# Kernel tuning notes

Hardware: AMD Instinct MI355X
Metric: run time of the kernel (lower is better)

The kernel has to match this reference:

```python
import jax, jax.numpy as jnp
import numpy as np

B, C, H, W = 4, 256, 96, 96
FOUT = 32
HW = H * W
N = HW // 2  # inside/outside pixel counts (50/50 mask)


def setup_inputs() -> dict:
    key = jax.random.key(0)
    ks = jax.random.split(key, 6)
    f = jax.random.normal(ks[0], (B, C, H, W), dtype=jnp.float32)
    # deterministic alternating mask -> fixed N_in = N_out = HW/2 (jit-friendly)
    flat = (jnp.arange(HW) % 2).astype(jnp.float32)
    mask = jnp.broadcast_to(flat.reshape(1, 1, H, W), (B, 1, H, W))
    idx_in = jnp.nonzero(flat > 0.5, size=N)[0].astype(jnp.int32)   # mask == 1
    idx_out = jnp.nonzero(flat < 0.5, size=N)[0].astype(jnp.int32)  # mask == 0
    scale = 0.02
    Wq = jax.random.normal(ks[1], (FOUT, C), dtype=jnp.float32) * scale
    Wk = jax.random.normal(ks[2], (FOUT, C), dtype=jnp.float32) * scale
    Wv = jax.random.normal(ks[3], (C, C), dtype=jnp.float32) * scale
    bq = jnp.zeros((FOUT,), jnp.float32)
    bk = jnp.zeros((FOUT,), jnp.float32)
    bv = jnp.zeros((C,), jnp.float32)
    gamma = jax.random.uniform(ks[4], (1,), dtype=jnp.float32) + 0.25  # nonzero
    return {"f": f, "mask": mask, "idx_out": idx_out, "idx_in": idx_in,
            "Wq": Wq, "bq": bq, "Wk": Wk, "bk": bk, "Wv": Wv, "bv": bv,
            "gamma": gamma}


def reference(f, mask, idx_out, idx_in, Wq, bq, Wk, bk, Wv, bv, gamma):
    b, c, h, w = f.shape
    ff = f.reshape(b, c, h * w)              # (b, c, hw)
    f_out_pix = ff[:, :, idx_out]            # (b, c, Nout) gather outside pixels
    f_in_pix = ff[:, :, idx_in]              # (b, c, Nin)  gather inside pixels
    # 1x1 convs on gathered pixel sets == per-pixel linear projections
    q = jnp.einsum('oc,bcn->bon', Wq, f_out_pix) + bq[None, :, None]  # (b, fout, Nout)
    k = jnp.einsum('oc,bcn->bon', Wk, f_in_pix) + bk[None, :, None]   # (b, fout, Nin)
    v = jnp.einsum('dc,bcn->bdn', Wv, f_in_pix) + bv[None, :, None]   # (b, c, Nin)
    energy = jnp.einsum('boq,bok->bqk', q, k)       # (b, Nout, Nin)
    att = jax.nn.softmax(energy, axis=-1)
    r_v = jnp.einsum('bck,bqk->bcq', v, att)        # (b, c, Nout)
    ff2 = ff.at[:, :, idx_out].set(r_v)             # scatter write-back
    f_reshape = ff2.reshape(b, c, h, w)
    # NOTE: in torch, f_in aliases f's storage and is mutated by the scatter,
    # so f_in == f_reshape here. Reproduce that aliasing faithfully.
    f_out = f_reshape * (1.0 - mask) * gamma + f_reshape
    return (f_reshape, f_out)
```

## Files before the change

### kernel.cpp

```cpp
#include <hip/hip_runtime.h>
#include <math.h>

#define B_DIM    4
#define C_DIM    256
#define HW_DIM   9216
#define N_PIX    4608
#define FOUT_DIM 32
#define L2E      1.44269504f

typedef float  f32x4  __attribute__((ext_vector_type(4)));
typedef short  bf16x8 __attribute__((ext_vector_type(8)));

static __device__ __forceinline__ unsigned short f2bf(float x) {
    union { float f; unsigned int u; } v; v.f = x;
    unsigned int r = v.u + 0x7fffu + ((v.u >> 16) & 1u);
    return (unsigned short)(r >> 16);
}
static __device__ __forceinline__ float bf2f(unsigned short u) {
    union { unsigned int u; float f; } v; v.u = (unsigned int)u << 16; return v.f;
}

static __device__ __forceinline__ void gload_lds16(const unsigned short* g, unsigned short* l) {
    __builtin_amdgcn_global_load_lds(
        (const __attribute__((address_space(1))) void*)g,
        (__attribute__((address_space(3))) void*)l, 16, 0, 0);
}

__global__ void inv_init(int* __restrict__ inv) {
    int i = blockIdx.x * 256 + threadIdx.x;
    if (i < HW_DIM) inv[i] = -1;
}
__global__ void inv_scatter(const int* __restrict__ idx_out, int* __restrict__ inv) {
    int i = blockIdx.x * 256 + threadIdx.x;
    if (i < N_PIX) inv[idx_out[i]] = i;
}

__global__ __launch_bounds__(256) void gather_f(
    const float* __restrict__ f, const int* __restrict__ idx_out, const int* __restrict__ idx_in,
    unsigned short* __restrict__ Fo, unsigned short* __restrict__ Fi) {
    __shared__ float Fs[2][32][65];
    __shared__ int io[64], ii[64];
    const int t = threadIdx.x;
    const int n0 = blockIdx.x * 64, c0 = blockIdx.y * 32, b = blockIdx.z;
    if (t < 64) { io[t] = idx_out[n0 + t]; ii[t] = idx_in[n0 + t]; }
    __syncthreads();
    const float* fb = f + (size_t)b * C_DIM * HW_DIM;
    const int nn = t & 63, cg = t >> 6;
#pragma unroll
    for (int i = 0; i < 8; i++) {
        int c = cg * 8 + i;
        Fs[0][c][nn] = fb[(size_t)(c0 + c) * HW_DIM + io[nn]];
        Fs[1][c][nn] = fb[(size_t)(c0 + c) * HW_DIM + ii[nn]];
    }
    __syncthreads();
    for (int r = t; r < 2048; r += 256) {
        int n = r >> 5, c = r & 31;
        size_t o = ((size_t)(b * N_PIX + n0 + n)) * C_DIM + c0 + c;
        Fo[o] = f2bf(Fs[0][c][n]);
        Fi[o] = f2bf(Fs[1][c][n]);
    }
}

#define FSP 40
__global__ __launch_bounds__(256) void qk_proj_mfma(
    const unsigned short* __restrict__ Fo, const unsigned short* __restrict__ Fi,
    const float* __restrict__ Wq, const float* __restrict__ bq,
    const float* __restrict__ Wk, const float* __restrict__ bk,
    unsigned short* __restrict__ Q, unsigned short* __restrict__ K) {
    __shared__ unsigned short Ws[32 * 264];
    __shared__ unsigned short Fs[256 * FSP];
    const int t = threadIdx.x, n0 = blockIdx.x * 256, sel = blockIdx.y, b = blockIdx.z;
    const unsigned short* FX = sel ? Fi : Fo;
    const float* W    = sel ? Wk : Wq;
    const float* bias = sel ? bk : bq;
    unsigned short* O = sel ? K : Q;
#pragma unroll
    for (int j = 0; j < 8; j++) {
        int fid = j * 256 + t, row = fid >> 6, f4 = fid & 63;
        float4 wv = *(const float4*)(W + (size_t)row * C_DIM + f4 * 4);
        uint2 pk;
        pk.x = f2bf(wv.x) | ((unsigned)f2bf(wv.y) << 16);
        pk.y = f2bf(wv.z) | ((unsigned)f2bf(wv.w) << 16);
        *(uint2*)(Ws + row * 264 + f4 * 4) = pk;
    }
    const int w = t >> 6, l = t & 63, lq = l & 15, lg = l >> 4;
    f32x4 acc[8];
#pragma unroll
    for (int i = 0; i < 8; i++) acc[i] = (f32x4){0.f, 0.f, 0.f, 0.f};
    for (int cs = 0; cs < 8; cs++) {
        __syncthreads();
#pragma unroll
        for (int j = 0; j < 4; j++) {
            int cid = j * 256 + t, row = cid >> 2, ch = cid & 3;
            *(uint4*)(Fs + row * FSP + ch * 8) =
                *(const uint4*)(FX + ((size_t)(b * N_PIX + n0 + row)) * C_DIM + cs * 32 + ch * 8);
        }
        __syncthreads();
        bf16x8 bfr[2];
#pragma unroll
        for (int ob = 0; ob < 2; ob++)
            bfr[ob] = *(const bf16x8*)(Ws + (ob * 16 + lq) * 264 + cs * 32 + lg * 8);
#pragma unroll
        for (int ab = 0; ab < 4; ab++) {
            bf16x8 a = *(const bf16x8*)(Fs + (w * 64 + ab * 16 + lq) * FSP + lg * 8);
#pragma unroll
            for (int ob = 0; ob < 2; ob++)
                acc[ab * 2 + ob] = __builtin_amdgcn_mfma_f32_16x16x32_bf16(a, bfr[ob], acc[ab * 2 + ob], 0, 0, 0);
        }
    }
#pragma unroll
    for (int ab = 0; ab < 4; ab++)
#pragma unroll
        for (int ob = 0; ob < 2; ob++)
#pragma unroll
            for (int r = 0; r < 4; r++) {
                int n = n0 + w * 64 + ab * 16 + lg * 4 + r;
                int o = ob * 16 + lq;
                O[((size_t)(b * N_PIX + n)) * FOUT_DIM + o] = f2bf(acc[ab * 2 + ob][r] + bias[o]);
            }
}

__global__ __launch_bounds__(256) void v_proj_mfma(
    const unsigned short* __restrict__ Fi, const float* __restrict__ Wv,
    const float* __restrict__ bv, unsigned short* __restrict__ VT) {
    __shared__ unsigned short Ws[128 * FSP];
    __shared__ unsigned short Fs[128 * FSP];
    const int t = threadIdx.x, n0 = blockIdx.x * 128, d0 = blockIdx.y * 128, b = blockIdx.z;
    const int w = t >> 6, wd = w & 1, wn = w >> 1, l = t & 63, lq = l & 15, lg = l >> 4;
    f32x4 acc[16];
#pragma unroll
    for (int i = 0; i < 16; i++) acc[i] = (f32x4){0.f, 0.f, 0.f, 0.f};
    for (int cs = 0; cs < 8; cs++) {
        __syncthreads();
#pragma unroll
        for (int j = 0; j < 4; j++) {
            int row = j * 32 + (t >> 3), f4 = t & 7;
            float4 wv = *(const float4*)(Wv + (size_t)(d0 + row) * C_DIM + cs * 32 + f4 * 4);
            uint2 pk;
            pk.x = f2bf(wv.x) | ((unsigned)f2bf(wv.y) << 16);
            pk.y = f2bf(wv.z) | ((unsigned)f2bf(wv.w) << 16);
            *(uint2*)(Ws + row * FSP + f4 * 4) = pk;
        }
#pragma unroll
        for (int j = 0; j < 2; j++) {
            int cid = j * 256 + t, row = cid >> 2, ch = cid & 3;
            *(uint4*)(Fs + row * FSP + ch * 8) =
                *(const uint4*)(Fi + ((size_t)(b * N_PIX + n0 + row)) * C_DIM + cs * 32 + ch * 8);
        }
        __syncthreads();
        bf16x8 bfr[4];
#pragma unroll
        for (int nb = 0; nb < 4; nb++)
            bfr[nb] = *(const bf16x8*)(Fs + (wn * 64 + nb * 16 + lq) * FSP + lg * 8);
#pragma unroll
        for (int ab = 0; ab < 4; ab++) {
            bf16x8 a = *(const bf16x8*)(Ws + (wd * 64 + ab * 16 + lq) * FSP + lg * 8);
#pragma unroll
            for (int nb = 0; nb < 4; nb++)
                acc[ab * 4 + nb] = __builtin_amdgcn_mfma_f32_16x16x32_bf16(a, bfr[nb], acc[ab * 4 + nb], 0, 0, 0);
        }
    }
#pragma unroll
    for (int ab = 0; ab < 4; ab++)
#pragma unroll
        for (int r = 0; r < 4; r++) {
            int d = d0 + wd * 64 + ab * 16 + lg * 4 + r;
            float bvv = bv[d];
#pragma unroll
            for (int nb = 0; nb < 4; nb++) {
                int n = n0 + wn * 64 + nb * 16 + lq;
                VT[((size_t)(b * C_DIM + d)) * N_PIX + n] = f2bf(acc[ab * 4 + nb][r] + bvv);
            }
        }
}

__global__ __launch_bounds__(256, 2) void flash_attn(
    const unsigned short* __restrict__ Q, const unsigned short* __restrict__ K,
    const unsigned short* __restrict__ VT,
    unsigned short* __restrict__ Rpart, float* __restrict__ lpart) {
    __shared__ __align__(16) unsigned short VB[256 * 64];
    __shared__ __align__(16) unsigned short PB[2][32 * 72];
    __shared__ float lred[2][2][2][16];
    const int t = threadIdx.x, w = t >> 6, l = t & 63, lq = l & 15, lg = l >> 4;
    const int qg = w & 1, dh = w >> 1;
    const int bid = blockIdx.x;
    const int bz = bid & 7, b = bz & 3, ks = bz >> 2;
    const int q0 = (bid >> 3) * 64 + qg * 32;
    const int d0 = dh * 128;
    const unsigned short* Qb = Q + (size_t)b * N_PIX * FOUT_DIM;
    const unsigned short* Kb = K + (size_t)b * N_PIX * FOUT_DIM;
    const unsigned short* Vb = VT + (size_t)b * C_DIM * N_PIX;
    unsigned short* Rp = Rpart + (size_t)ks * 4718592;
    float* lp = lpart + ks * (B_DIM * N_PIX);

    bf16x8 qfr[2];
    qfr[0] = *(const bf16x8*)(Qb + (size_t)(q0 + lq) * 32 + lg * 8);
    qfr[1] = *(const bf16x8*)(Qb + (size_t)(q0 + 16 + lq) * 32 + lg * 8);

    f32x4 acc[2][8];
#pragma unroll
    for (int qb = 0; qb < 2; qb++)
#pragma unroll
        for (int db = 0; db < 8; db++) acc[qb][db] = (f32x4){0.f, 0.f, 0.f, 0.f};
    float lsum[2] = {0.f, 0.f};

    int voff[8];
#pragma unroll
    for (int j = 0; j < 8; j++) {
        int row = (w * 8 + j) * 8 + (l >> 3);
        int ch  = (l & 7) ^ (row & 7);
        voff[j] = row * N_PIX + ch * 8;
    }
    const int kt0 = ks * 36;
    bf16x8 kpf[2];
    {
        int kg = kt0 * 64;
#pragma unroll
        for (int j = 0; j < 8; j++)
            gload_lds16(Vb + voff[j] + kg, VB + (w * 8 + j) * 512);
#pragma unroll
        for (int kb = 0; kb < 2; kb++)
            kpf[kb] = *(const bf16x8*)(Kb + (size_t)(kg + dh * 32 + kb * 16 + lq) * 32 + lg * 8);
    }

    const int swz = lq & 7;
#pragma unroll 1
    for (int it = 0; it < 36; it++) {
        {
            const f32x4 z4 = {0.f, 0.f, 0.f, 0.f};
#pragma unroll
            for (int qb = 0; qb < 2; qb++) {
                f32x4 s[2];
#pragma unroll
                for (int kb = 0; kb < 2; kb++)
                    s[kb] = __builtin_amdgcn_mfma_f32_16x16x32_bf16(kpf[kb], qfr[qb], z4, 0, 0, 0);
                float ps = 0.f;
#pragma unroll
                for (int kb = 0; kb < 2; kb++) {
                    float p0 = exp2f(s[kb][0] * L2E);
                    float p1 = exp2f(s[kb][1] * L2E);
                    float p2 = exp2f(s[kb][2] * L2E);
                    float p3 = exp2f(s[kb][3] * L2E);
                    ps += (p0 + p1) + (p2 + p3);
                    unsigned int u0 = (__float_as_uint(p0) + 0x8000u) >> 16;
                    unsigned int u1 = (__float_as_uint(p1) + 0x8000u) & 0xffff0000u;
                    unsigned int u2 = (__float_as_uint(p2) + 0x8000u) >> 16;
                    unsigned int u3 = (__float_as_uint(p3) + 0x8000u) & 0xffff0000u;
                    uint2 pk; pk.x = u0 | u1; pk.y = u2 | u3;
                    *(uint2*)(PB[qg] + (qb * 16 + lq) * 72 + dh * 32 + kb * 16 + lg * 4) = pk;
                }
                lsum[qb] += ps;
            }
        }
        __syncthreads();
        if (it + 1 < 36) {
            int kn = (kt0 + it + 1) * 64;
#pragma unroll
            for (int kb = 0; kb < 2; kb++)
                kpf[kb] = *(const bf16x8*)(Kb + (size_t)(kn + dh * 32 + kb * 16 + lq) * 32 + lg * 8);
        }
        bf16x8 af[2][2];
#pragma unroll
        for (int qb = 0; qb < 2; qb++) {
            af[qb][0] = *(const bf16x8*)(PB[qg] + (qb * 16 + lq) * 72 + lg * 8);
            af[qb][1] = *(const bf16x8*)(PB[qg] + (qb * 16 + lq) * 72 + 32 + lg * 8);
        }
#pragma unroll
        for (int db = 0; db < 8; db++) {
            int row = d0 + db * 16 + lq;
            bf16x8 b0 = *(const bf16x8*)(VB + row * 64 + (lg ^ swz) * 8);
            bf16x8 b1 = *(const bf16x8*)(VB + row * 64 + ((lg + 4) ^ swz) * 8);
#pragma unroll
            for (int qb = 0; qb < 2; qb++) {
                acc[qb][db] = __builtin_amdgcn_mfma_f32_16x16x32_bf16(af[qb][0], b0, acc[qb][db], 0, 0, 0);
                acc[qb][db] = __builtin_amdgcn_mfma_f32_16x16x32_bf16(af[qb][1], b1, acc[qb][db], 0, 0, 0);
            }
        }
        __syncthreads();
        if (it + 1 < 36) {
            int kn = (kt0 + it + 1) * 64;
#pragma unroll
            for (int j = 0; j < 8; j++)
                gload_lds16(Vb + voff[j] + kn, VB + (w * 8 + j) * 512);
        }
    }
#pragma unroll
    for (int qb = 0; qb < 2; qb++)
#pragma unroll
        for (int r = 0; r < 4; r++) {
            int q = q0 + qb * 16 + lg * 4 + r;
            unsigned short* rp = Rp + ((size_t)(b * N_PIX + q)) * C_DIM + d0;
#pragma unroll
            for (int db = 0; db < 8; db++)
                rp[db * 16 + lq] = f2bf(acc[qb][db][r]);
        }
#pragma unroll
    for (int qb = 0; qb < 2; qb++) {
        float v = lsum[qb];
        v += __shfl_xor(v, 16);
        v += __shfl_xor(v, 32);
        if (l < 16) lred[dh][qg][qb][l] = v;
    }
    __syncthreads();
    if (dh == 0 && l < 16) {
#pragma unroll
        for (int qb = 0; qb < 2; qb++)
            lp[b * N_PIX + q0 + qb * 16 + l] = lred[0][qg][qb][l] + lred[1][qg][qb][l];
    }
}

__global__ __launch_bounds__(256) void epilogue(
    const float* __restrict__ f, const float* __restrict__ mask,
    const unsigned short* __restrict__ R0, const unsigned short* __restrict__ R1,
    const float* __restrict__ l0, const float* __restrict__ l1,
    const int* __restrict__ inv, const float* __restrict__ gamma,
    float* __restrict__ out0, float* __restrict__ out1) {
    const int gid = blockIdx.x * 256 + threadIdx.x;
    const size_t e = (size_t)gid * 4;
    const int p = (int)(e % HW_DIM);
    const int bc = (int)(e / HW_DIM);
    const int b = bc >> 8;
    const int c = bc & 255;
    const float g = gamma[0];
    float4 fv = *(const float4*)(f + e);
    const float* fvp = (const float*)&fv;
    float o0[4], o1[4];
#pragma unroll
    for (int u = 0; u < 4; u++) {
        int pp = p + u;
        int n = inv[pp];
        float val;
        if (n >= 0) {
            size_t ri = ((size_t)(b * N_PIX + n)) * C_DIM + c;
            float s = bf2f(R0[ri]) + bf2f(R1[ri]);
            val = s / (l0[b * N_PIX + n] + l1[b * N_PIX + n]);
        } else {
            val = fvp[u];
        }
        float mv = mask[b * HW_DIM + pp];
        o0[u] = val;
        o1[u] = val * (1.0f + g * (1.0f - mv));
    }
    *(float4*)(out0 + e) = make_float4(o0[0], o0[1], o0[2], o0[3]);
    *(float4*)(out1 + e) = make_float4(o1[0], o1[1], o1[2], o1[3]);
}

extern "C" void kernel_launch(void* const* d_in, const int* in_sizes, int n_in,
                              void* d_out, int out_size, void* d_ws, size_t ws_size,
                              hipStream_t stream) {
    const float* f       = (const float*)d_in[0];
    const float* mask    = (const float*)d_in[1];
    const int*   idx_out = (const int*)d_in[2];
    const int*   idx_in  = (const int*)d_in[3];
    const float* Wq      = (const float*)d_in[4];
    const float* bq      = (const float*)d_in[5];
    const float* Wk      = (const float*)d_in[6];
    const float* bk      = (const float*)d_in[7];
    const float* Wv      = (const float*)d_in[8];
    const float* bv      = (const float*)d_in[9];
    const float* gamma   = (const float*)d_in[10];

    unsigned short* ws   = (unsigned short*)d_ws;
    unsigned short* Fo   = ws;
    unsigned short* Fi   = ws + 4718592;
    unsigned short* VTw  = ws + 9437184;
    unsigned short* Qw   = ws + 14155776;
    unsigned short* Kw   = ws + 14745600;
    float*          lptr = (float*)(ws + 15335424);
    int*            inv  = (int*)(lptr + 2 * B_DIM * N_PIX);
    unsigned short* Rpart = Fo;

    float* out0 = (float*)d_out;
    float* out1 = out0 + (size_t)B_DIM * C_DIM * HW_DIM;

    inv_init<<<dim3(36), dim3(256), 0, stream>>>(inv);
    inv_scatter<<<dim3(18), dim3(256), 0, stream>>>(idx_out, inv);
    gather_f<<<dim3(72, 8, B_DIM), dim3(256), 0, stream>>>(f, idx_out, idx_in, Fo, Fi);
    qk_proj_mfma<<<dim3(18, 2, B_DIM), dim3(256), 0, stream>>>(Fo, Fi, Wq, bq, Wk, bk, Qw, Kw);
    v_proj_mfma<<<dim3(36, 2, B_DIM), dim3(256), 0, stream>>>(Fi, Wv, bv, VTw);
    flash_attn<<<dim3(576), dim3(256), 0, stream>>>(Qw, Kw, VTw, Rpart, lptr);
    epilogue<<<dim3(9216), dim3(256), 0, stream>>>(f, mask, Rpart, Rpart + 4718592,
                                                   lptr, lptr + B_DIM * N_PIX, inv, gamma, out0, out1);
}
```

Baseline: 285.5 us.

## Fuse Q/K/V projections and inverse-index build into one launch; vectorize gather stores

Merges the Q/K projection, V projection and inverse-index construction kernels into a single block-indexed 'prep' kernel, which cuts four launches down to one and lets the independent work run concurrently. The inverse-index init no longer fills the whole table with -1. It now writes -1 only at idx_in positions, which assumes idx_in and idx_out together cover every pixel. The gather kernel now writes 8 bf16 values per thread as one 16-byte store instead of scalar 2-byte stores. The trade-offs are a larger shared-memory footprint per block and branch divergence across block roles.

```diff
diff --git a/kernel.cpp b/kernel.cpp
--- a/kernel.cpp
+++ b/kernel.cpp
@@ -24,15 +24,6 @@
     __builtin_amdgcn_global_load_lds(
         (const __attribute__((address_space(1))) void*)g,
         (__attribute__((address_space(3))) void*)l, 16, 0, 0);
-}
-
-__global__ void inv_init(int* __restrict__ inv) {
-    int i = blockIdx.x * 256 + threadIdx.x;
-    if (i < HW_DIM) inv[i] = -1;
-}
-__global__ void inv_scatter(const int* __restrict__ idx_out, int* __restrict__ inv) {
-    int i = blockIdx.x * 256 + threadIdx.x;
-    if (i < N_PIX) inv[idx_out[i]] = i;
 }
 
 __global__ __launch_bounds__(256) void gather_f(
@@ -53,125 +44,142 @@
         Fs[1][c][nn] = fb[(size_t)(c0 + c) * HW_DIM + ii[nn]];
     }
     __syncthreads();
-    for (int r = t; r < 2048; r += 256) {
-        int n = r >> 5, c = r & 31;
-        size_t o = ((size_t)(b * N_PIX + n0 + n)) * C_DIM + c0 + c;
-        Fo[o] = f2bf(Fs[0][c][n]);
-        Fi[o] = f2bf(Fs[1][c][n]);
+    {
+        const int n = t >> 2, oc = (t & 3) * 8;
+        size_t o = ((size_t)(b * N_PIX + n0 + n)) * C_DIM + c0 + oc;
+        unsigned short tmp0[8], tmp1[8];
+#pragma unroll
+        for (int j = 0; j < 8; j++) {
+            tmp0[j] = f2bf(Fs[0][oc + j][n]);
+            tmp1[j] = f2bf(Fs[1][oc + j][n]);
+        }
+        *(uint4*)(Fo + o) = *(uint4*)tmp0;
+        *(uint4*)(Fi + o) = *(uint4*)tmp1;
     }
 }
 
 #define FSP 40
-__global__ __launch_bounds__(256) void qk_proj_mfma(
+__global__ __launch_bounds__(256) void prep(
     const unsigned short* __restrict__ Fo, const unsigned short* __restrict__ Fi,
     const float* __restrict__ Wq, const float* __restrict__ bq,
     const float* __restrict__ Wk, const float* __restrict__ bk,
-    unsigned short* __restrict__ Q, unsigned short* __restrict__ K) {
-    __shared__ unsigned short Ws[32 * 264];
-    __shared__ unsigned short Fs[256 * FSP];
-    const int t = threadIdx.x, n0 = blockIdx.x * 256, sel = blockIdx.y, b = blockIdx.z;
-    const unsigned short* FX = sel ? Fi : Fo;
-    const float* W    = sel ? Wk : Wq;
-    const float* bias = sel ? bk : bq;
-    unsigned short* O = sel ? K : Q;
-#pragma unroll
-    for (int j = 0; j < 8; j++) {
-        int fid = j * 256 + t, row = fid >> 6, f4 = fid & 63;
-        float4 wv = *(const float4*)(W + (size_t)row * C_DIM + f4 * 4);
-        uint2 pk;
-        pk.x = f2bf(wv.x) | ((unsigned)f2bf(wv.y) << 16);
-        pk.y = f2bf(wv.z) | ((unsigned)f2bf(wv.w) << 16);
-        *(uint2*)(Ws + row * 264 + f4 * 4) = pk;
-    }
-    const int w = t >> 6, l = t & 63, lq = l & 15, lg = l >> 4;
-    f32x4 acc[8];
-#pragma unroll
-    for (int i = 0; i < 8; i++) acc[i] = (f32x4){0.f, 0.f, 0.f, 0.f};
-    for (int cs = 0; cs < 8; cs++) {
-        __syncthreads();
-#pragma unroll
-        for (int j = 0; j < 4; j++) {
-            int cid = j * 256 + t, row = cid >> 2, ch = cid & 3;
-            *(uint4*)(Fs + row * FSP + ch * 8) =
-                *(const uint4*)(FX + ((size_t)(b * N_PIX + n0 + row)) * C_DIM + cs * 32 + ch * 8);
-        }
-        __syncthreads();
-        bf16x8 bfr[2];
-#pragma unroll
-        for (int ob = 0; ob < 2; ob++)
-            bfr[ob] = *(const bf16x8*)(Ws + (ob * 16 + lq) * 264 + cs * 32 + lg * 8);
-#pragma unroll
-        for (int ab = 0; ab < 4; ab++) {
-            bf16x8 a = *(const bf16x8*)(Fs + (w * 64 + ab * 16 + lq) * FSP + lg * 8);
-#pragma unroll
-            for (int ob = 0; ob < 2; ob++)
-                acc[ab * 2 + ob] = __builtin_amdgcn_mfma_f32_16x16x32_bf16(a, bfr[ob], acc[ab * 2 + ob], 0, 0, 0);
-        }
-    }
-#pragma unroll
-    for (int ab = 0; ab < 4; ab++)
-#pragma unroll
-        for (int ob = 0; ob < 2; ob++)
-#pragma unroll
-            for (int r = 0; r < 4; r++) {
-                int n = n0 + w * 64 + ab * 16 + lg * 4 + r;
-                int o = ob * 16 + lq;
-                O[((size_t)(b * N_PIX + n)) * FOUT_DIM + o] = f2bf(acc[ab * 2 + ob][r] + bias[o]);
-            }
-}
-
-__global__ __launch_bounds__(256) void v_proj_mfma(
-    const unsigned short* __restrict__ Fi, const float* __restrict__ Wv,
-    const float* __restrict__ bv, unsigned short* __restrict__ VT) {
-    __shared__ unsigned short Ws[128 * FSP];
-    __shared__ unsigned short Fs[128 * FSP];
-    const int t = threadIdx.x, n0 = blockIdx.x * 128, d0 = blockIdx.y * 128, b = blockIdx.z;
-    const int w = t >> 6, wd = w & 1, wn = w >> 1, l = t & 63, lq = l & 15, lg = l >> 4;
-    f32x4 acc[16];
-#pragma unroll
-    for (int i = 0; i < 16; i++) acc[i] = (f32x4){0.f, 0.f, 0.f, 0.f};
-    for (int cs = 0; cs < 8; cs++) {
-        __syncthreads();
-#pragma unroll
-        for (int j = 0; j < 4; j++) {
-            int row = j * 32 + (t >> 3), f4 = t & 7;
-            float4 wv = *(const float4*)(Wv + (size_t)(d0 + row) * C_DIM + cs * 32 + f4 * 4);
+    const float* __restrict__ Wv, const float* __restrict__ bv,
+    unsigned short* __restrict__ Q, unsigned short* __restrict__ K,
+    unsigned short* __restrict__ VT,
+    const int* __restrict__ idx_out, const int* __restrict__ idx_in,
+    int* __restrict__ inv) {
+    __shared__ __align__(16) unsigned short SM[18688];
+    const int bid = blockIdx.x, t = threadIdx.x;
+    if (bid < 144) {
+        unsigned short* Ws = SM;
+        unsigned short* Fs = SM + 8448;
+        const int n0 = (bid % 18) * 256, sel = (bid / 18) & 1, b = bid / 36;
+        const unsigned short* FX = sel ? Fi : Fo;
+        const float* W    = sel ? Wk : Wq;
+        const float* bias = sel ? bk : bq;
+        unsigned short* O = sel ? K : Q;
+#pragma unroll
+        for (int j = 0; j < 8; j++) {
+            int fid = j * 256 + t, row = fid >> 6, f4 = fid & 63;
+            float4 wv = *(const float4*)(W + (size_t)row * C_DIM + f4 * 4);
             uint2 pk;
             pk.x = f2bf(wv.x) | ((unsigned)f2bf(wv.y) << 16);
             pk.y = f2bf(wv.z) | ((unsigned)f2bf(wv.w) << 16);
-            *(uint2*)(Ws + row * FSP + f4 * 4) = pk;
-        }
-#pragma unroll
-        for (int j = 0; j < 2; j++) {
-            int cid = j * 256 + t, row = cid >> 2, ch = cid & 3;
-            *(uint4*)(Fs + row * FSP + ch * 8) =
-                *(const uint4*)(Fi + ((size_t)(b * N_PIX + n0 + row)) * C_DIM + cs * 32 + ch * 8);
-        }
-        __syncthreads();
-        bf16x8 bfr[4];
-#pragma unroll
-        for (int nb = 0; nb < 4; nb++)
-            bfr[nb] = *(const bf16x8*)(Fs + (wn * 64 + nb * 16 + lq) * FSP + lg * 8);
-#pragma unroll
-        for (int ab = 0; ab < 4; ab++) {
-            bf16x8 a = *(const bf16x8*)(Ws + (wd * 64 + ab * 16 + lq) * FSP + lg * 8);
+            *(uint2*)(Ws + row * 264 + f4 * 4) = pk;
+        }
+        const int w = t >> 6, l = t & 63, lq = l & 15, lg = l >> 4;
+        f32x4 acc[8];
+#pragma unroll
+        for (int i = 0; i < 8; i++) acc[i] = (f32x4){0.f, 0.f, 0.f, 0.f};
+        for (int cs = 0; cs < 8; cs++) {
+            __syncthreads();
+#pragma unroll
+            for (int j = 0; j < 4; j++) {
+                int cid = j * 256 + t, row = cid >> 2, ch = cid & 3;
+                *(uint4*)(Fs + row * FSP + ch * 8) =
+                    *(const uint4*)(FX + ((size_t)(b * N_PIX + n0 + row)) * C_DIM + cs * 32 + ch * 8);
+            }
+            __syncthreads();
+            bf16x8 bfr[2];
+#pragma unroll
+            for (int ob = 0; ob < 2; ob++)
+                bfr[ob] = *(const bf16x8*)(Ws + (ob * 16 + lq) * 264 + cs * 32 + lg * 8);
+#pragma unroll
+            for (int ab = 0; ab < 4; ab++) {
+                bf16x8 a = *(const bf16x8*)(Fs + (w * 64 + ab * 16 + lq) * FSP + lg * 8);
+#pragma unroll
+                for (int ob = 0; ob < 2; ob++)
+                    acc[ab * 2 + ob] = __builtin_amdgcn_mfma_f32_16x16x32_bf16(a, bfr[ob], acc[ab * 2 + ob], 0, 0, 0);
+            }
+        }
+#pragma unroll
+        for (int ab = 0; ab < 4; ab++)
+#pragma unroll
+            for (int ob = 0; ob < 2; ob++)
+#pragma unroll
+                for (int r = 0; r < 4; r++) {
+                    int n = n0 + w * 64 + ab * 16 + lg * 4 + r;
+                    int o = ob * 16 + lq;
+                    O[((size_t)(b * N_PIX + n)) * FOUT_DIM + o] = f2bf(acc[ab * 2 + ob][r] + bias[o]);
+                }
+    } else if (bid < 432) {
+        unsigned short* Ws = SM;
+        unsigned short* Fs = SM + 5120;
+        const int vb = bid - 144;
+        const int n0 = (vb % 36) * 128, d0 = ((vb / 36) & 1) * 128, b = vb / 72;
+        const int w = t >> 6, wd = w & 1, wn = w >> 1, l = t & 63, lq = l & 15, lg = l >> 4;
+        f32x4 acc[16];
+#pragma unroll
+        for (int i = 0; i < 16; i++) acc[i] = (f32x4){0.f, 0.f, 0.f, 0.f};
+        for (int cs = 0; cs < 8; cs++) {
+            __syncthreads();
+#pragma unroll
+            for (int j = 0; j < 4; j++) {
+                int row = j * 32 + (t >> 3), f4 = t & 7;
+                float4 wv = *(const float4*)(Wv + (size_t)(d0 + row) * C_DIM + cs * 32 + f4 * 4);
+                uint2 pk;
+                pk.x = f2bf(wv.x) | ((unsigned)f2bf(wv.y) << 16);
+                pk.y = f2bf(wv.z) | ((unsigned)f2bf(wv.w) << 16);
+                *(uint2*)(Ws + row * FSP + f4 * 4) = pk;
+            }
+#pragma unroll
+            for (int j = 0; j < 2; j++) {
+                int cid = j * 256 + t, row = cid >> 2, ch = cid & 3;
+                *(uint4*)(Fs + row * FSP + ch * 8) =
+                    *(const uint4*)(Fi + ((size_t)(b * N_PIX + n0 + row)) * C_DIM + cs * 32 + ch * 8);
+            }
+            __syncthreads();
+            bf16x8 bfr[4];
 #pragma unroll
             for (int nb = 0; nb < 4; nb++)
-                acc[ab * 4 + nb] = __builtin_amdgcn_mfma_f32_16x16x32_bf16(a, bfr[nb], acc[ab * 4 + nb], 0, 0, 0);
-        }
-    }
-#pragma unroll
-    for (int ab = 0; ab < 4; ab++)
-#pragma unroll
-        for (int r = 0; r < 4; r++) {
-            int d = d0 + wd * 64 + ab * 16 + lg * 4 + r;
-            float bvv = bv[d];
-#pragma unroll
-            for (int nb = 0; nb < 4; nb++) {
-                int n = n0 + wn * 64 + nb * 16 + lq;
-                VT[((size_t)(b * C_DIM + d)) * N_PIX + n] = f2bf(acc[ab * 4 + nb][r] + bvv);
-            }
-        }
+                bfr[nb] = *(const bf16x8*)(Fs + (wn * 64 + nb * 16 + lq) * FSP + lg * 8);
+#pragma unroll
+            for (int ab = 0; ab < 4; ab++) {
+                bf16x8 a = *(const bf16x8*)(Ws + (wd * 64 + ab * 16 + lq) * FSP + lg * 8);
+#pragma unroll
+                for (int nb = 0; nb < 4; nb++)
+                    acc[ab * 4 + nb] = __builtin_amdgcn_mfma_f32_16x16x32_bf16(a, bfr[nb], acc[ab * 4 + nb], 0, 0, 0);
+            }
+        }
+#pragma unroll
+        for (int ab = 0; ab < 4; ab++)
+#pragma unroll
+            for (int r = 0; r < 4; r++) {
+                int d = d0 + wd * 64 + ab * 16 + lg * 4 + r;
+                float bvv = bv[d];
+#pragma unroll
+                for (int nb = 0; nb < 4; nb++) {
+                    int n = n0 + wn * 64 + nb * 16 + lq;
+                    VT[((size_t)(b * C_DIM + d)) * N_PIX + n] = f2bf(acc[ab * 4 + nb][r] + bvv);
+                }
+            }
+    } else {
+        int i = (bid - 432) * 256 + t;
+        if (i < N_PIX) {
+            inv[idx_out[i]] = i;
+            inv[idx_in[i]] = -1;
+        }
+    }
 }
 
 __global__ __launch_bounds__(256, 2) void flash_attn(
@@ -373,11 +381,9 @@
     float* out0 = (float*)d_out;
     float* out1 = out0 + (size_t)B_DIM * C_DIM * HW_DIM;
 
-    inv_init<<<dim3(36), dim3(256), 0, stream>>>(inv);
-    inv_scatter<<<dim3(18), dim3(256), 0, stream>>>(idx_out, inv);
     gather_f<<<dim3(72, 8, B_DIM), dim3(256), 0, stream>>>(f, idx_out, idx_in, Fo, Fi);
-    qk_proj_mfma<<<dim3(18, 2, B_DIM), dim3(256), 0, stream>>>(Fo, Fi, Wq, bq, Wk, bk, Qw, Kw);
-    v_proj_mfma<<<dim3(36, 2, B_DIM), dim3(256), 0, stream>>>(Fi, Wv, bv, VTw);
+    prep<<<dim3(450), dim3(256), 0, stream>>>(Fo, Fi, Wq, bq, Wk, bk, Wv, bv,
+                                              Qw, Kw, VTw, idx_out, idx_in, inv);
     flash_attn<<<dim3(576), dim3(256), 0, stream>>>(Qw, Kw, VTw, Rpart, lptr);
     epilogue<<<dim3(9216), dim3(256), 0, stream>>>(f, mask, Rpart, Rpart + 4718592,
                                                    lptr, lptr + B_DIM * N_PIX, inv, gamma, out0, out1);
```

After: 268.4 us. -6.0%, faster.
